# Kernel tuning notes

Measured on AMD Instinct MI355X. Metric: run time of the kernel, lower is better.

Reference implementation:

```python
import jax, jax.numpy as jnp
import numpy as np

N = 10000
E = 160000
IN_DIM = 128
HID = 128
HEADS = 8
INT_DIM = 512
OUT_DIM = 3
NEG_SLOPE = 0.2


def gat_conv(x, src, dst, W, a_src, a_dst, b, heads, ch):
    # x: [N, F_in]; W: [F_in, heads*ch]; a_src/a_dst: [heads, ch]; b: [heads*ch]
    n = x.shape[0]
    h = (x @ W).reshape(n, heads, ch)                      # [N,H,C]
    alpha_src = jnp.einsum('nhc,hc->nh', h, a_src)         # [N,H]
    alpha_dst = jnp.einsum('nhc,hc->nh', h, a_dst)         # [N,H]
    e = jax.nn.leaky_relu(alpha_src[src] + alpha_dst[dst], NEG_SLOPE)  # [E,H]
    # segment softmax over incoming edges of each dst node
    emax = jax.ops.segment_max(e, dst, num_segments=n)     # [N,H]
    ee = jnp.exp(e - emax[dst])
    denom = jax.ops.segment_sum(ee, dst, num_segments=n)   # [N,H]
    alpha = ee / (denom[dst] + 1e-16)                      # [E,H]
    msg = h[src] * alpha[:, :, None]                       # [E,H,C]
    out = jax.ops.segment_sum(msg, dst, num_segments=n)    # [N,H,C]
    return out.reshape(n, heads * ch) + b


def setup_inputs() -> dict:
    key = jax.random.key(0)
    ks = jax.random.split(key, 20)

    def glorot(k, shape):
        fan = shape[0] + shape[-1]
        s = jnp.sqrt(6.0 / fan)
        return jax.random.uniform(k, shape, jnp.float32, -s, s)

    x = jax.random.normal(ks[0], (N, IN_DIM), jnp.float32)
    edge_index = jax.random.randint(ks[1], (2, E), 0, N, jnp.int32)
    return {
        'x': x,
        'edge_index': edge_index,
        'W1': glorot(ks[2], (IN_DIM, HEADS * HID)),
        'a_src1': glorot(ks[3], (HEADS, HID)),
        'a_dst1': glorot(ks[4], (HEADS, HID)),
        'b1': jnp.zeros((HEADS * HID,), jnp.float32),
        'W2': glorot(ks[5], (HEADS * HID, HEADS * HID)),
        'a_src2': glorot(ks[6], (HEADS, HID)),
        'a_dst2': glorot(ks[7], (HEADS, HID)),
        'b2': jnp.zeros((HEADS * HID,), jnp.float32),
        'W3': glorot(ks[8], (HEADS * HID, INT_DIM)),
        'a_src3': glorot(ks[9], (1, INT_DIM)),
        'a_dst3': glorot(ks[10], (1, INT_DIM)),
        'b3': jnp.zeros((INT_DIM,), jnp.float32),
        'Wl': glorot(ks[11], (INT_DIM, INT_DIM)),
        'bl': jnp.zeros((INT_DIM,), jnp.float32),
        'Wc': glorot(ks[12], (INT_DIM, OUT_DIM)),
        'bc': jnp.zeros((OUT_DIM,), jnp.float32),
    }


def reference(x, edge_index, W1, a_src1, a_dst1, b1, W2, a_src2, a_dst2, b2,
              W3, a_src3, a_dst3, b3, Wl, bl, Wc, bc):
    src, dst = edge_index[0], edge_index[1]
    # eval mode: dropout_edge and Dropout are identity
    h = gat_conv(x, src, dst, W1, a_src1, a_dst1, b1, HEADS, HID)
    h = jax.nn.relu(h)
    h = gat_conv(h, src, dst, W2, a_src2, a_dst2, b2, HEADS, HID)
    h = jax.nn.relu(h)
    h = gat_conv(h, src, dst, W3, a_src3, a_dst3, b3, 1, INT_DIM)
    h = jax.nn.relu(h)
    h = jax.nn.relu(h @ Wl + bl)
    return h @ Wc + bc
```

## Files before the change

kernel.cpp:

```cpp
#include <hip/hip_runtime.h>
#include <hip/hip_bf16.h>

#define NN 10000
#define EE 160000
#define IN_DIM 128
#define HID 128
#define HEADS 8
#define F1 (HEADS*HID)
#define INT_DIM 512
#define OUT_DIM 3
#define MPAD 10112

typedef __attribute__((ext_vector_type(4))) float f32x4;
typedef __attribute__((ext_vector_type(8))) _Float16 half8;
typedef __attribute__((ext_vector_type(4))) _Float16 half4;
typedef __attribute__((ext_vector_type(2))) _Float16 half2v;

#define WAVE_SYNC() do { asm volatile("s_waitcnt lgkmcnt(0)" ::: "memory"); \
                         __builtin_amdgcn_sched_barrier(0); } while(0)

__global__ __launch_bounds__(256) void count_kernel(const int* __restrict__ dst, int E, int* __restrict__ cnt){
    int e = blockIdx.x*256 + threadIdx.x;
    if(e < E) atomicAdd(&cnt[dst[e]], 1);
}

__global__ __launch_bounds__(256) void scan_kernel(const int* __restrict__ cnt, int* __restrict__ rowp,
                                                   int* __restrict__ cursor, int n){
    __shared__ int sh[256];
    __shared__ int stotal;
    int t = threadIdx.x;
    if(t==0) stotal = 0;
    __syncthreads();
    for(int base=0; base<n; base+=256){
        int i = base + t;
        int v = (i<n) ? cnt[i] : 0;
        sh[t] = v;
        __syncthreads();
        #pragma unroll
        for(int off=1; off<256; off<<=1){
            int add = (t>=off) ? sh[t-off] : 0;
            __syncthreads();
            sh[t] += add;
            __syncthreads();
        }
        int excl = sh[t] - v;
        if(i<n){ rowp[i] = stotal + excl; cursor[i] = stotal + excl; }
        int chunk_total = sh[255];
        __syncthreads();
        if(t==0) stotal += chunk_total;
        __syncthreads();
    }
    if(t==0) rowp[n] = stotal;
}

__global__ __launch_bounds__(256) void fill_kernel(const int* __restrict__ src, const int* __restrict__ dst,
                                                   int E, int* __restrict__ cursor, int* __restrict__ colsrc){
    int e = blockIdx.x*256 + threadIdx.x;
    if(e < E){
        int d = dst[e];
        int pos = atomicAdd(&cursor[d], 1);
        colsrc[pos] = src[e];
    }
}

__global__ __launch_bounds__(256) void splitT16_kernel(const float* __restrict__ B, _Float16* __restrict__ T,
                                                       int K, int N){
    __shared__ float tile[32][33];
    const int tx = threadIdx.x & 31, ty = threadIdx.x >> 5;
    const int n0 = blockIdx.x * 32, k0 = blockIdx.y * 32;
    #pragma unroll
    for(int i = 0; i < 32; i += 8)
        tile[ty + i][tx] = B[(size_t)(k0 + ty + i) * N + n0 + tx];
    __syncthreads();
    #pragma unroll
    for(int i = 0; i < 32; i += 8){
        int n = ty + i;
        T[(size_t)(n0 + n) * K + k0 + tx] = (_Float16)tile[tx][n];
    }
}

__global__ __launch_bounds__(256) void x16_kernel(const float* __restrict__ x, _Float16* __restrict__ x16, int n4){
    int i = blockIdx.x*256 + threadIdx.x;
    if(i >= n4) return;
    float4 v = ((const float4*)x)[i];
    half4 o = { (_Float16)v.x, (_Float16)v.y, (_Float16)v.z, (_Float16)v.w };
    ((half4*)x16)[i] = o;
}

__global__ __launch_bounds__(256) void aw1_kernel(const float* __restrict__ W1,
                                                  const float* __restrict__ a_src,
                                                  const float* __restrict__ a_dst,
                                                  float* __restrict__ aw){
    int idx = blockIdx.x*256 + threadIdx.x;
    if(idx >= 16*IN_DIM) return;
    int j = idx >> 7, k = idx & 127;
    int hj = j & 7;
    const float* av = (j < 8 ? a_src : a_dst) + hj*HID;
    const float* wr = W1 + (size_t)k*F1 + hj*HID;
    float s = 0.f;
    #pragma unroll 4
    for(int c = 0; c < HID; c++) s += av[c] * wr[c];
    aw[idx] = s;
}

__global__ __launch_bounds__(256) void alpha1_kernel(const float* __restrict__ x,
                                                     const float* __restrict__ aw,
                                                     float* __restrict__ asrc, float* __restrict__ adst){
    __shared__ float xs[16][128];
    __shared__ float aws[16][128];
    int t = threadIdx.x;
    int nb = blockIdx.x * 16;
    for(int i = t; i < 16*128; i += 256){
        xs[i >> 7][i & 127] = x[(size_t)nb*128 + i];
        aws[i >> 7][i & 127] = aw[i];
    }
    __syncthreads();
    int nl = t >> 4, j = t & 15;
    float s = 0.f;
    #pragma unroll 4
    for(int c = 0; c < 128; c++) s += xs[nl][c] * aws[j][c];
    int node = nb + nl;
    if(j < 8) asrc[node*8 + j] = s;
    else      adst[node*8 + (j-8)] = s;
}

__global__ __launch_bounds__(256) void agg1_kernel(const _Float16* __restrict__ x16,
                                                   const float* __restrict__ asrc,
                                                   const float* __restrict__ adst,
                                                   const int* __restrict__ rowp,
                                                   const int* __restrict__ colsrc,
                                                   _Float16* __restrict__ oa){
    const int w = threadIdx.x >> 6, l = threadIdx.x & 63;
    const int node = blockIdx.x*4 + w;
    __shared__ float sh_ee[4][64][8];
    int beg = rowp[node], end = rowp[node+1];
    float rd = adst[node*8 + (l & 7)];
    float acc0[8], acc1[8];
    #pragma unroll
    for(int h=0;h<8;h++){ acc0[h]=0.f; acc1[h]=0.f; }
    float dpart = 0.f;
    for(int base=beg; base<end; base+=64){
        int clen = min(64, end-base);
        WAVE_SYNC();
        int sreg = (l < clen) ? colsrc[base + l] : 0;
        for(int it=l; it<clen*8; it+=64){
            int j = it >> 3;
            int s = colsrc[base + j];
            float e = asrc[s*8 + (l & 7)] + rd;
            e = (e > 0.f) ? e : 0.2f*e;
            float ee = expf(e);
            sh_ee[w][j][l & 7] = ee;
            dpart += ee;
        }
        WAVE_SYNC();
        #pragma unroll 2
        for(int j=0;j<clen;j++){
            int s = __shfl(sreg, j);
            half2v xv = ((const half2v*)(x16 + (size_t)s*128))[l];
            float x0 = (float)xv[0], x1 = (float)xv[1];
            #pragma unroll
            for(int h=0;h<8;h++){
                float wt = sh_ee[w][j][h];
                acc0[h] += wt * x0;
                acc1[h] += wt * x1;
            }
        }
    }
    dpart += __shfl_xor(dpart, 8);
    dpart += __shfl_xor(dpart, 16);
    dpart += __shfl_xor(dpart, 32);
    #pragma unroll
    for(int h=0;h<8;h++){
        float dn = __shfl(dpart, h) + 1e-16f;
        half2v o = { (_Float16)(acc0[h]/dn), (_Float16)(acc1[h]/dn) };
        *(half2v*)(oa + (size_t)node*F1 + h*128 + 2*l) = o;
    }
}

__device__ inline void fma8x2(float* acc, half8 v0, half8 v1, float w0, float w1){
    #pragma unroll
    for(int k=0;k<8;k++){
        acc[k]   += w0 * (float)v0[k];
        acc[8+k] += w1 * (float)v1[k];
    }
}
__device__ inline void fma8(float* acc, half8 v, float w){
    #pragma unroll
    for(int k=0;k<8;k++) acc[k] += w * (float)v[k];
}

__global__ __launch_bounds__(256) void agg2_kernel(const _Float16* __restrict__ hbuf,
                                                   const float* __restrict__ asrc,
                                                   const float* __restrict__ adst,
                                                   const int* __restrict__ rowp,
                                                   const int* __restrict__ colsrc,
                                                   const float* __restrict__ bias,
                                                   _Float16* __restrict__ oa){
    const int w = threadIdx.x >> 6, l = threadIdx.x & 63;
    const int node = blockIdx.x*4 + w;
    __shared__ float sh_ee[4][64][8];
    int beg = rowp[node], end = rowp[node+1];
    float rd = adst[node*8 + (l & 7)];
    float acc[16];
    #pragma unroll
    for(int k=0;k<16;k++) acc[k]=0.f;
    float dpart = 0.f;
    for(int base=beg; base<end; base+=64){
        int clen = min(64, end-base);
        int cpad = (clen + 3) & ~3;
        WAVE_SYNC();
        int sreg = (l < clen) ? colsrc[base + l] : 0;
        #pragma unroll 1
        for(int it=l; it<cpad*8; it+=64){
            int j = it >> 3;
            float ee = 0.f;
            if(j < clen){
                int s = colsrc[base + j];
                float e = asrc[s*8 + (l & 7)] + rd;
                e = (e > 0.f) ? e : 0.2f*e;
                ee = expf(e);
                dpart += ee;
            }
            sh_ee[w][j][l & 7] = ee;
        }
        WAVE_SYNC();
        int sA=__shfl(sreg,0), sB=__shfl(sreg,1), sC=__shfl(sreg,2), sD=__shfl(sreg,3);
        const half8* pA=(const half8*)(hbuf+(size_t)sA*F1);
        const half8* pB=(const half8*)(hbuf+(size_t)sB*F1);
        const half8* pC=(const half8*)(hbuf+(size_t)sC*F1);
        const half8* pD=(const half8*)(hbuf+(size_t)sD*F1);
        half8 vA0=pA[l], vA1=pA[l+64];
        half8 vB0=pB[l], vB1=pB[l+64];
        half8 vC0=pC[l], vC1=pC[l+64];
        half8 vD0=pD[l], vD1=pD[l+64];
        const int h0 = l>>4, h1 = 4 + (l>>4);
        #pragma unroll 1
        for(int j0=0; j0<cpad; j0+=4){
            half8 nA0,nA1,nB0,nB1,nC0,nC1,nD0,nD1;
            const bool more = (j0+4 < cpad);
            if(more){
                int t0=__shfl(sreg,j0+4), t1=__shfl(sreg,j0+5), t2=__shfl(sreg,j0+6), t3=__shfl(sreg,j0+7);
                const half8* q0=(const half8*)(hbuf+(size_t)t0*F1);
                const half8* q1=(const half8*)(hbuf+(size_t)t1*F1);
                const half8* q2=(const half8*)(hbuf+(size_t)t2*F1);
                const half8* q3=(const half8*)(hbuf+(size_t)t3*F1);
                nA0=q0[l]; nA1=q0[l+64];
                nB0=q1[l]; nB1=q1[l+64];
                nC0=q2[l]; nC1=q2[l+64];
                nD0=q3[l]; nD1=q3[l+64];
            }
            fma8x2(acc, vA0, vA1, sh_ee[w][j0  ][h0], sh_ee[w][j0  ][h1]);
            fma8x2(acc, vB0, vB1, sh_ee[w][j0+1][h0], sh_ee[w][j0+1][h1]);
            fma8x2(acc, vC0, vC1, sh_ee[w][j0+2][h0], sh_ee[w][j0+2][h1]);
            fma8x2(acc, vD0, vD1, sh_ee[w][j0+3][h0], sh_ee[w][j0+3][h1]);
            if(more){
                vA0=nA0; vA1=nA1; vB0=nB0; vB1=nB1;
                vC0=nC0; vC1=nC1; vD0=nD0; vD1=nD1;
            }
        }
    }
    dpart += __shfl_xor(dpart, 8);
    dpart += __shfl_xor(dpart, 16);
    dpart += __shfl_xor(dpart, 32);
    float dn0 = __shfl(dpart, l>>4) + 1e-16f;
    float dn1 = __shfl(dpart, 4 + (l>>4)) + 1e-16f;
    const float4* bp = (const float4*)bias;
    float4 ba0 = bp[2*l],       ba1 = bp[2*l+1];
    float4 bc0 = bp[128 + 2*l], bc1 = bp[128 + 2*l+1];
    float bb0[8] = {ba0.x,ba0.y,ba0.z,ba0.w, ba1.x,ba1.y,ba1.z,ba1.w};
    float bb1[8] = {bc0.x,bc0.y,bc0.z,bc0.w, bc1.x,bc1.y,bc1.z,bc1.w};
    half8 o0, o1;
    #pragma unroll
    for(int k=0;k<8;k++){
        o0[k] = (_Float16)fmaxf(acc[k]/dn0 + bb0[k], 0.f);
        o1[k] = (_Float16)fmaxf(acc[8+k]/dn1 + bb1[k], 0.f);
    }
    size_t off0 = (size_t)node*F1 + 8*l;
    *(half8*)(oa + off0) = o0;
    *(half8*)(oa + off0 + 512) = o1;
}

__global__ __launch_bounds__(256) void agg3_kernel(const _Float16* __restrict__ hbuf,
                                                   const float* __restrict__ asrc,
                                                   const float* __restrict__ adst,
                                                   const int* __restrict__ rowp,
                                                   const int* __restrict__ colsrc,
                                                   const float* __restrict__ bias,
                                                   _Float16* __restrict__ oa){
    const int w = threadIdx.x >> 6, l = threadIdx.x & 63;
    const int node = blockIdx.x*4 + w;
    int beg = rowp[node], end = rowp[node+1];
    float rd = adst[node];
    float acc[8];
    #pragma unroll
    for(int k=0;k<8;k++) acc[k]=0.f;
    float dpart = 0.f;
    for(int base=beg; base<end; base+=64){
        int clen = min(64, end-base);
        int sreg = 0; float eereg = 0.f;
        if(l < clen){
            sreg = colsrc[base + l];
            float e = asrc[sreg] + rd;
            e = (e > 0.f) ? e : 0.2f*e;
            eereg = expf(e);
            dpart += eereg;
        }
        int cpad = (clen + 7) & ~7;
        half8 v[8];
        float wt[8];
        #pragma unroll
        for(int k=0;k<8;k++){
            int s = __shfl(sreg, k);
            wt[k] = __shfl(eereg, k);
            v[k] = ((const half8*)(hbuf + (size_t)s*INT_DIM))[l];
        }
        #pragma unroll 1
        for(int j0=0; j0<cpad; j0+=8){
            half8 nv[8]; float nw[8];
            const bool more = (j0+8 < cpad);
            if(more){
                #pragma unroll
                for(int k=0;k<8;k++){
                    int s = __shfl(sreg, j0+8+k);
                    nw[k] = __shfl(eereg, j0+8+k);
                    nv[k] = ((const half8*)(hbuf + (size_t)s*INT_DIM))[l];
                }
            }
            #pragma unroll
            for(int k=0;k<8;k++) fma8(acc, v[k], wt[k]);
            if(more){
                #pragma unroll
                for(int k=0;k<8;k++){ v[k]=nv[k]; wt[k]=nw[k]; }
            }
        }
    }
    #pragma unroll
    for(int off=1; off<64; off<<=1) dpart += __shfl_xor(dpart, off);
    float dn = dpart + 1e-16f;
    const float4* bp = (const float4*)bias;
    float4 ba0 = bp[2*l], ba1 = bp[2*l+1];
    float bb[8] = {ba0.x,ba0.y,ba0.z,ba0.w, ba1.x,ba1.y,ba1.z,ba1.w};
    half8 o;
    #pragma unroll
    for(int k=0;k<8;k++)
        o[k] = (_Float16)fmaxf(acc[k]/dn + bb[k], 0.f);
    *(half8*)(oa + (size_t)node*INT_DIM + 8*l) = o;
}

template<int FUSE>
__global__ __launch_bounds__(512, 4) void mfma16_gemm_kernel(
    const _Float16* __restrict__ A, int lda, int za,
    const _Float16* __restrict__ B, int ldb, int zb,
    const float* __restrict__ bias, _Float16* __restrict__ O,
    int ldc, int zc, int K, int gx)
{
    __shared__ _Float16 lA[2][128*32];
    __shared__ _Float16 lB[2][128*32];
    const int tid  = threadIdx.x;
    const int lane = tid & 63;
    const int w    = tid >> 6;
    const int wm   = w >> 2;
    const int wn   = w & 3;
    const int z    = blockIdx.z;

    const int nwg = gridDim.x;
    const int q = nwg >> 3, r = nwg & 7;
    const int xcd = blockIdx.x & 7, idx = blockIdx.x >> 3;
    const int wgid = (xcd < r ? xcd*(q+1) : r*(q+1) + (xcd-r)*q) + idx;
    const int row0 = (wgid / gx) * 128, col0 = (wgid % gx) * 128;

    f32x4 acc[4][2];
    #pragma unroll
    for(int i=0;i<4;i++)
        #pragma unroll
        for(int j=0;j<2;j++) acc[i][j] = (f32x4){0.f,0.f,0.f,0.f};

    const int rr1 = tid >> 2;
    const int ss1 = (tid & 3) ^ ((rr1 >> 1) & 3);
    const size_t aoff = (size_t)(row0 + rr1) * lda + (size_t)z*za + ss1 * 8;
    const size_t boff = (size_t)(col0 + rr1) * ldb + (size_t)z*zb + ss1 * 8;

    typedef __attribute__((address_space(3))) char lds_char;
    lds_char* dA = (lds_char*)(&lA[0][0]) + w*1024;
    lds_char* dB = (lds_char*)(&lB[0][0]) + w*1024;

    int arow[4], brow[2];
    const int slotx = ((lane >> 4) ^ ((lane >> 1) & 3)) << 4;
    #pragma unroll
    for(int i=0;i<4;i++)
        arow[i] = (wm*64 + i*16 + (lane & 15)) * 64 + slotx;
    #pragma unroll
    for(int j=0;j<2;j++)
        brow[j] = (wn*32 + j*16 + (lane & 15)) * 64 + slotx;

    #define GLDS(src, dst) __builtin_amdgcn_global_load_lds( \
        (__attribute__((address_space(1))) void*)(src), \
        (__attribute__((address_space(3))) void*)(dst), 16, 0, 0)
    GLDS(A + aoff, dA);
    GLDS(B + boff, dB);
    __syncthreads();

    #pragma unroll 1
    for(int k0 = 0, kb = 0; k0 < K; k0 += 32, kb ^= 1){
        if(k0 + 32 < K){
            const int nb = kb ^ 1;
            GLDS(A + aoff + k0 + 32, dA + nb*8192);
            GLDS(B + boff + k0 + 32, dB + nb*8192);
        }
        const char* pA = (const char*)(&lA[0][0]) + kb*8192;
        const char* pB = (const char*)(&lB[0][0]) + kb*8192;
        half8 af[4];
        #pragma unroll
        for(int i=0;i<4;i++) af[i] = *(const half8*)(pA + arow[i]);
        #pragma unroll
        for(int j=0;j<2;j++){
            half8 bf = *(const half8*)(pB + brow[j]);
            #pragma unroll
            for(int i=0;i<4;i++)
                acc[i][j] = __builtin_amdgcn_mfma_f32_16x16x32_f16(af[i], bf, acc[i][j], 0, 0, 0);
        }
        __syncthreads();
    }
    #undef GLDS

    #pragma unroll
    for(int i=0;i<4;i++){
        const int rr = row0 + wm*64 + i*16 + ((lane >> 4) << 2);
        #pragma unroll
        for(int j=0;j<2;j++){
            const int gc = z*zc + col0 + wn*32 + j*16 + (lane & 15);
            float b = FUSE ? bias[gc] : 0.f;
            #pragma unroll
            for(int rg=0;rg<4;rg++){
                float v = acc[i][j][rg];
                if(FUSE) v = fmaxf(v + b, 0.f);
                O[(size_t)(rr + rg) * ldc + gc] = (_Float16)v;
            }
        }
    }
}

__global__ __launch_bounds__(128) void alpha16_h8_kernel(const _Float16* __restrict__ hbuf,
                                                         const float* __restrict__ a_src,
                                                         const float* __restrict__ a_dst,
                                                         float* __restrict__ asrc, float* __restrict__ adst){
    int node = blockIdx.x;
    int t = threadIdx.x;
    half8 v = ((const half8*)(hbuf + (size_t)node*F1))[t];
    const float4* ap = (const float4*)(a_src + 8*t);
    const float4* dp = (const float4*)(a_dst + 8*t);
    float4 a0 = ap[0], a1 = ap[1];
    float4 d0 = dp[0], d1 = dp[1];
    float av[8] = {a0.x,a0.y,a0.z,a0.w, a1.x,a1.y,a1.z,a1.w};
    float dv[8] = {d0.x,d0.y,d0.z,d0.w, d1.x,d1.y,d1.z,d1.w};
    float ps = 0.f, pd = 0.f;
    #pragma unroll
    for(int k=0;k<8;k++){
        float f = (float)v[k];
        ps += f * av[k];
        pd += f * dv[k];
    }
    #pragma unroll
    for(int off=8; off; off>>=1){ ps += __shfl_down(ps, off); pd += __shfl_down(pd, off); }
    if((t & 15) == 0){
        asrc[(size_t)node*8 + (t>>4)] = ps;
        adst[(size_t)node*8 + (t>>4)] = pd;
    }
}

__global__ __launch_bounds__(128) void alpha16_h1_kernel(const _Float16* __restrict__ hbuf,
                                                         const float* __restrict__ a_src,
                                                         const float* __restrict__ a_dst,
                                                         float* __restrict__ asrc, float* __restrict__ adst){
    int node = blockIdx.x;
    int t = threadIdx.x;
    half4 v = ((const half4*)(hbuf + (size_t)node*INT_DIM))[t];
    float4 a = ((const float4*)a_src)[t];
    float4 d = ((const float4*)a_dst)[t];
    float ps = (float)v[0]*a.x + (float)v[1]*a.y + (float)v[2]*a.z + (float)v[3]*a.w;
    float pd = (float)v[0]*d.x + (float)v[1]*d.y + (float)v[2]*d.z + (float)v[3]*d.w;
    #pragma unroll
    for(int off=32; off; off>>=1){ ps += __shfl_down(ps, off); pd += __shfl_down(pd, off); }
    __shared__ float shs[2], shd[2];
    int wv = t >> 6;
    if((t & 63) == 0){ shs[wv] = ps; shd[wv] = pd; }
    __syncthreads();
    if(t == 0){
        asrc[node] = shs[0] + shs[1];
        adst[node] = shd[0] + shd[1];
    }
}

__global__ __launch_bounds__(256) void cls16_kernel(const _Float16* __restrict__ h, const float* __restrict__ Wc,
                                                    const float* __restrict__ bc, float* __restrict__ out, int n){
    int node = blockIdx.x*4 + (threadIdx.x >> 6);
    int lane = threadIdx.x & 63;
    if(node >= n) return;
    half8 v = ((const half8*)(h + (size_t)node*INT_DIM))[lane];
    float s0=0.f, s1=0.f, s2=0.f;
    #pragma unroll
    for(int k=0;k<8;k++){
        float f = (float)v[k];
        const float* wr = Wc + (8*lane + k)*3;
        s0 += f * wr[0];
        s1 += f * wr[1];
        s2 += f * wr[2];
    }
    #pragma unroll
    for(int off=32; off; off>>=1){
        s0 += __shfl_down(s0, off);
        s1 += __shfl_down(s1, off);
        s2 += __shfl_down(s2, off);
    }
    if(lane==0){
        out[(size_t)node*3+0] = s0 + bc[0];
        out[(size_t)node*3+1] = s1 + bc[1];
        out[(size_t)node*3+2] = s2 + bc[2];
    }
}

extern "C" void kernel_launch(void* const* d_in, const int* in_sizes, int n_in,
                              void* d_out, int out_size, void* d_ws, size_t ws_size,
                              hipStream_t stream){
    const float* x      = (const float*)d_in[0];
    const int*   ei     = (const int*)d_in[1];
    const float* W1     = (const float*)d_in[2];
    const float* a_src1 = (const float*)d_in[3];
    const float* a_dst1 = (const float*)d_in[4];
    const float* b1     = (const float*)d_in[5];
    const float* W2     = (const float*)d_in[6];
    const float* a_src2 = (const float*)d_in[7];
    const float* a_dst2 = (const float*)d_in[8];
    const float* b2     = (const float*)d_in[9];
    const float* W3     = (const float*)d_in[10];
    const float* a_src3 = (const float*)d_in[11];
    const float* a_dst3 = (const float*)d_in[12];
    const float* b3     = (const float*)d_in[13];
    const float* Wl     = (const float*)d_in[14];
    const float* bl     = (const float*)d_in[15];
    const float* Wc     = (const float*)d_in[16];
    const float* bc     = (const float*)d_in[17];
    float* out = (float*)d_out;

    const int* src = ei;
    const int* dst = ei + EE;

    char* p = (char*)d_ws;
    char* regA = p;  p += (size_t)MPAD*F1*4;
    char* regB = p;  p += (size_t)MPAD*F1*4;
    _Float16* wt16 = (_Float16*)p;  p += (size_t)F1*F1*2;
    _Float16* x16  = (_Float16*)p;  p += (size_t)NN*IN_DIM*2;
    float* aw1  = (float*)p;  p += 16*IN_DIM*4;
    float* asrc = (float*)p;  p += (size_t)NN*HEADS*4;
    float* adst = (float*)p;  p += (size_t)NN*HEADS*4;
    int* cnt    = (int*)p;    p += NN*4;
    int* rowp   = (int*)p;    p += (NN+1)*4;
    int* cursor = (int*)p;    p += NN*4;
    int* colsrc = (int*)p;    p += EE*4;

    _Float16* hA = (_Float16*)regA;
    _Float16* hB = (_Float16*)regB;

    hipMemsetAsync(cnt, 0, NN*sizeof(int), stream);
    count_kernel<<<(EE+255)/256, 256, 0, stream>>>(dst, EE, cnt);
    scan_kernel<<<1, 256, 0, stream>>>(cnt, rowp, cursor, NN);
    fill_kernel<<<(EE+255)/256, 256, 0, stream>>>(src, dst, EE, cursor, colsrc);

    x16_kernel<<<(NN*IN_DIM/4 + 255)/256, 256, 0, stream>>>(x, x16, NN*IN_DIM/4);
    splitT16_kernel<<<dim3(F1/32, IN_DIM/32), 256, 0, stream>>>(W1, wt16, IN_DIM, F1);
    aw1_kernel<<<8, 256, 0, stream>>>(W1, a_src1, a_dst1, aw1);
    alpha1_kernel<<<NN/16, 256, 0, stream>>>(x, aw1, asrc, adst);
    agg1_kernel<<<NN/4, 256, 0, stream>>>(x16, asrc, adst, rowp, colsrc, hA);
    mfma16_gemm_kernel<1><<<dim3(MPAD/128, 1, HEADS), 512, 0, stream>>>(
        hA, F1, 128,  wt16, IN_DIM, 128*IN_DIM,
        b1, hB, F1, 128,  IN_DIM, 1);

    splitT16_kernel<<<dim3(F1/32, F1/32), 256, 0, stream>>>(W2, wt16, F1, F1);
    mfma16_gemm_kernel<0><<<dim3((F1/128)*(MPAD/128), 1, 1), 512, 0, stream>>>(
        hB, F1, 0,  wt16, F1, 0,
        nullptr, hA, F1, 0,  F1, F1/128);
    alpha16_h8_kernel<<<NN, 128, 0, stream>>>(hA, a_src2, a_dst2, asrc, adst);
    agg2_kernel<<<NN/4, 256, 0, stream>>>(hA, asrc, adst, rowp, colsrc, b2, hB);

    splitT16_kernel<<<dim3(INT_DIM/32, F1/32), 256, 0, stream>>>(W3, wt16, F1, INT_DIM);
    mfma16_gemm_kernel<0><<<dim3((INT_DIM/128)*(MPAD/128), 1, 1), 512, 0, stream>>>(
        hB, F1, 0,  wt16, F1, 0,
        nullptr, hA, INT_DIM, 0,  F1, INT_DIM/128);
    alpha16_h1_kernel<<<NN, 128, 0, stream>>>(hA, a_src3, a_dst3, asrc, adst);
    agg3_kernel<<<NN/4, 256, 0, stream>>>(hA, asrc, adst, rowp, colsrc, b3, hB);

    splitT16_kernel<<<dim3(INT_DIM/32, INT_DIM/32), 256, 0, stream>>>(Wl, wt16, INT_DIM, INT_DIM);
    mfma16_gemm_kernel<1><<<dim3((INT_DIM/128)*(MPAD/128), 1, 1), 512, 0, stream>>>(
        hB, INT_DIM, 0,  wt16, INT_DIM, 0,
        bl, hA, INT_DIM, 0,  INT_DIM, INT_DIM/128);

    cls16_kernel<<<(NN+3)/4, 256, 0, stream>>>(hA, Wc, bc, out, NN);
}
```

Measured before the change: 297.5 us.

## Split agg2/agg3 aggregation across feature chunks per block for more parallelism

The layer-2 and layer-3 aggregation kernels now assign one 128-feature chunk (a head for agg2, a quarter of the 512 features for agg3) to each block, and each lane handles two features. This launches eight times as many waves, which gives more memory-level parallelism for the gather-bound neighbour loads and cuts per-thread register use. In exchange, the edge-score computation (colsrc, asrc, exp) is repeated once per chunk, and each gather load shrinks to 4 bytes per lane, which may lower per-request efficiency.

```diff
diff --git a/kernel.cpp b/kernel.cpp
--- a/kernel.cpp
+++ b/kernel.cpp
@@ -177,18 +177,6 @@
     }
 }
 
-__device__ inline void fma8x2(float* acc, half8 v0, half8 v1, float w0, float w1){
-    #pragma unroll
-    for(int k=0;k<8;k++){
-        acc[k]   += w0 * (float)v0[k];
-        acc[8+k] += w1 * (float)v1[k];
-    }
-}
-__device__ inline void fma8(float* acc, half8 v, float w){
-    #pragma unroll
-    for(int k=0;k<8;k++) acc[k] += w * (float)v[k];
-}
-
 __global__ __launch_bounds__(256) void agg2_kernel(const _Float16* __restrict__ hbuf,
                                                    const float* __restrict__ asrc,
                                                    const float* __restrict__ adst,
@@ -197,87 +185,62 @@
                                                    const float* __restrict__ bias,
                                                    _Float16* __restrict__ oa){
     const int w = threadIdx.x >> 6, l = threadIdx.x & 63;
-    const int node = blockIdx.x*4 + w;
-    __shared__ float sh_ee[4][64][8];
+    const int h = blockIdx.x & 7;
+    const int node = (blockIdx.x >> 3)*4 + w;
     int beg = rowp[node], end = rowp[node+1];
-    float rd = adst[node*8 + (l & 7)];
-    float acc[16];
-    #pragma unroll
-    for(int k=0;k<16;k++) acc[k]=0.f;
+    float rd = adst[node*8 + h];
+    float acc0 = 0.f, acc1 = 0.f;
     float dpart = 0.f;
+    const _Float16* hb = hbuf + h*128 + 2*l;
     for(int base=beg; base<end; base+=64){
         int clen = min(64, end-base);
-        int cpad = (clen + 3) & ~3;
-        WAVE_SYNC();
-        int sreg = (l < clen) ? colsrc[base + l] : 0;
+        int sreg = 0; float eereg = 0.f;
+        if(l < clen){
+            sreg = colsrc[base + l];
+            float e = asrc[sreg*8 + h] + rd;
+            e = (e > 0.f) ? e : 0.2f*e;
+            eereg = expf(e);
+            dpart += eereg;
+        }
+        int cpad = (clen + 7) & ~7;
+        half2v v[8]; float wt[8];
+        #pragma unroll
+        for(int k=0;k<8;k++){
+            int s = __shfl(sreg, k);
+            wt[k] = __shfl(eereg, k);
+            v[k] = *(const half2v*)(hb + (size_t)s*F1);
+        }
         #pragma unroll 1
-        for(int it=l; it<cpad*8; it+=64){
-            int j = it >> 3;
-            float ee = 0.f;
-            if(j < clen){
-                int s = colsrc[base + j];
-                float e = asrc[s*8 + (l & 7)] + rd;
-                e = (e > 0.f) ? e : 0.2f*e;
-                ee = expf(e);
-                dpart += ee;
-            }
-            sh_ee[w][j][l & 7] = ee;
-        }
-        WAVE_SYNC();
-        int sA=__shfl(sreg,0), sB=__shfl(sreg,1), sC=__shfl(sreg,2), sD=__shfl(sreg,3);
-        const half8* pA=(const half8*)(hbuf+(size_t)sA*F1);
-        const half8* pB=(const half8*)(hbuf+(size_t)sB*F1);
-        const half8* pC=(const half8*)(hbuf+(size_t)sC*F1);
-        const half8* pD=(const half8*)(hbuf+(size_t)sD*F1);
-        half8 vA0=pA[l], vA1=pA[l+64];
-        half8 vB0=pB[l], vB1=pB[l+64];
-        half8 vC0=pC[l], vC1=pC[l+64];
-        half8 vD0=pD[l], vD1=pD[l+64];
-        const int h0 = l>>4, h1 = 4 + (l>>4);
-        #pragma unroll 1
-        for(int j0=0; j0<cpad; j0+=4){
-            half8 nA0,nA1,nB0,nB1,nC0,nC1,nD0,nD1;
-            const bool more = (j0+4 < cpad);
+        for(int j0=0; j0<cpad; j0+=8){
+            half2v nv[8]; float nw[8];
+            const bool more = (j0+8 < cpad);
             if(more){
-                int t0=__shfl(sreg,j0+4), t1=__shfl(sreg,j0+5), t2=__shfl(sreg,j0+6), t3=__shfl(sreg,j0+7);
-                const half8* q0=(const half8*)(hbuf+(size_t)t0*F1);
-                const half8* q1=(const half8*)(hbuf+(size_t)t1*F1);
-                const half8* q2=(const half8*)(hbuf+(size_t)t2*F1);
-                const half8* q3=(const half8*)(hbuf+(size_t)t3*F1);
-                nA0=q0[l]; nA1=q0[l+64];
-                nB0=q1[l]; nB1=q1[l+64];
-                nC0=q2[l]; nC1=q2[l+64];
-                nD0=q3[l]; nD1=q3[l+64];
-            }
-            fma8x2(acc, vA0, vA1, sh_ee[w][j0  ][h0], sh_ee[w][j0  ][h1]);
-            fma8x2(acc, vB0, vB1, sh_ee[w][j0+1][h0], sh_ee[w][j0+1][h1]);
-            fma8x2(acc, vC0, vC1, sh_ee[w][j0+2][h0], sh_ee[w][j0+2][h1]);
-            fma8x2(acc, vD0, vD1, sh_ee[w][j0+3][h0], sh_ee[w][j0+3][h1]);
+                #pragma unroll
+                for(int k=0;k<8;k++){
+                    int s = __shfl(sreg, j0+8+k);
+                    nw[k] = __shfl(eereg, j0+8+k);
+                    nv[k] = *(const half2v*)(hb + (size_t)s*F1);
+                }
+            }
+            #pragma unroll
+            for(int k=0;k<8;k++){
+                acc0 += wt[k]*(float)v[k][0];
+                acc1 += wt[k]*(float)v[k][1];
+            }
             if(more){
-                vA0=nA0; vA1=nA1; vB0=nB0; vB1=nB1;
-                vC0=nC0; vC1=nC1; vD0=nD0; vD1=nD1;
-            }
-        }
-    }
-    dpart += __shfl_xor(dpart, 8);
-    dpart += __shfl_xor(dpart, 16);
-    dpart += __shfl_xor(dpart, 32);
-    float dn0 = __shfl(dpart, l>>4) + 1e-16f;
-    float dn1 = __shfl(dpart, 4 + (l>>4)) + 1e-16f;
-    const float4* bp = (const float4*)bias;
-    float4 ba0 = bp[2*l],       ba1 = bp[2*l+1];
-    float4 bc0 = bp[128 + 2*l], bc1 = bp[128 + 2*l+1];
-    float bb0[8] = {ba0.x,ba0.y,ba0.z,ba0.w, ba1.x,ba1.y,ba1.z,ba1.w};
-    float bb1[8] = {bc0.x,bc0.y,bc0.z,bc0.w, bc1.x,bc1.y,bc1.z,bc1.w};
-    half8 o0, o1;
-    #pragma unroll
-    for(int k=0;k<8;k++){
-        o0[k] = (_Float16)fmaxf(acc[k]/dn0 + bb0[k], 0.f);
-        o1[k] = (_Float16)fmaxf(acc[8+k]/dn1 + bb1[k], 0.f);
-    }
-    size_t off0 = (size_t)node*F1 + 8*l;
-    *(half8*)(oa + off0) = o0;
-    *(half8*)(oa + off0 + 512) = o1;
+                #pragma unroll
+                for(int k=0;k<8;k++){ v[k]=nv[k]; wt[k]=nw[k]; }
+            }
+        }
+    }
+    #pragma unroll
+    for(int off=1; off<64; off<<=1) dpart += __shfl_xor(dpart, off);
+    float dn = dpart + 1e-16f;
+    const int f = h*128 + 2*l;
+    float2 bb = *(const float2*)(bias + f);
+    half2v o = { (_Float16)fmaxf(acc0/dn + bb.x, 0.f),
+                 (_Float16)fmaxf(acc1/dn + bb.y, 0.f) };
+    *(half2v*)(oa + (size_t)node*F1 + f) = o;
 }
 
 __global__ __launch_bounds__(256) void agg3_kernel(const _Float16* __restrict__ hbuf,
@@ -288,13 +251,14 @@
                                                    const float* __restrict__ bias,
                                                    _Float16* __restrict__ oa){
     const int w = threadIdx.x >> 6, l = threadIdx.x & 63;
-    const int node = blockIdx.x*4 + w;
+    const int i = blockIdx.x & 7;
+    const int chunk = i & 3, sub = i >> 2;
+    const int node = ((blockIdx.x >> 3)*2 + sub)*4 + w;
     int beg = rowp[node], end = rowp[node+1];
     float rd = adst[node];
-    float acc[8];
-    #pragma unroll
-    for(int k=0;k<8;k++) acc[k]=0.f;
+    float acc0 = 0.f, acc1 = 0.f;
     float dpart = 0.f;
+    const _Float16* hb = hbuf + chunk*128 + 2*l;
     for(int base=beg; base<end; base+=64){
         int clen = min(64, end-base);
         int sreg = 0; float eereg = 0.f;
@@ -306,28 +270,30 @@
             dpart += eereg;
         }
         int cpad = (clen + 7) & ~7;
-        half8 v[8];
-        float wt[8];
+        half2v v[8]; float wt[8];
         #pragma unroll
         for(int k=0;k<8;k++){
             int s = __shfl(sreg, k);
             wt[k] = __shfl(eereg, k);
-            v[k] = ((const half8*)(hbuf + (size_t)s*INT_DIM))[l];
+            v[k] = *(const half2v*)(hb + (size_t)s*INT_DIM);
         }
         #pragma unroll 1
         for(int j0=0; j0<cpad; j0+=8){
-            half8 nv[8]; float nw[8];
+            half2v nv[8]; float nw[8];
             const bool more = (j0+8 < cpad);
             if(more){
                 #pragma unroll
                 for(int k=0;k<8;k++){
                     int s = __shfl(sreg, j0+8+k);
                     nw[k] = __shfl(eereg, j0+8+k);
-                    nv[k] = ((const half8*)(hbuf + (size_t)s*INT_DIM))[l];
+                    nv[k] = *(const half2v*)(hb + (size_t)s*INT_DIM);
                 }
             }
             #pragma unroll
-            for(int k=0;k<8;k++) fma8(acc, v[k], wt[k]);
+            for(int k=0;k<8;k++){
+                acc0 += wt[k]*(float)v[k][0];
+                acc1 += wt[k]*(float)v[k][1];
+            }
             if(more){
                 #pragma unroll
                 for(int k=0;k<8;k++){ v[k]=nv[k]; wt[k]=nw[k]; }
@@ -337,14 +303,11 @@
     #pragma unroll
     for(int off=1; off<64; off<<=1) dpart += __shfl_xor(dpart, off);
     float dn = dpart + 1e-16f;
-    const float4* bp = (const float4*)bias;
-    float4 ba0 = bp[2*l], ba1 = bp[2*l+1];
-    float bb[8] = {ba0.x,ba0.y,ba0.z,ba0.w, ba1.x,ba1.y,ba1.z,ba1.w};
-    half8 o;
-    #pragma unroll
-    for(int k=0;k<8;k++)
-        o[k] = (_Float16)fmaxf(acc[k]/dn + bb[k], 0.f);
-    *(half8*)(oa + (size_t)node*INT_DIM + 8*l) = o;
+    const int f = chunk*128 + 2*l;
+    float2 bb = *(const float2*)(bias + f);
+    half2v o = { (_Float16)fmaxf(acc0/dn + bb.x, 0.f),
+                 (_Float16)fmaxf(acc1/dn + bb.y, 0.f) };
+    *(half2v*)(oa + (size_t)node*INT_DIM + f) = o;
 }
 
 template<int FUSE>
@@ -580,14 +543,14 @@
         hB, F1, 0,  wt16, F1, 0,
         nullptr, hA, F1, 0,  F1, F1/128);
     alpha16_h8_kernel<<<NN, 128, 0, stream>>>(hA, a_src2, a_dst2, asrc, adst);
-    agg2_kernel<<<NN/4, 256, 0, stream>>>(hA, asrc, adst, rowp, colsrc, b2, hB);
+    agg2_kernel<<<(NN/4)*8, 256, 0, stream>>>(hA, asrc, adst, rowp, colsrc, b2, hB);
 
     splitT16_kernel<<<dim3(INT_DIM/32, F1/32), 256, 0, stream>>>(W3, wt16, F1, INT_DIM);
     mfma16_gemm_kernel<0><<<dim3((INT_DIM/128)*(MPAD/128), 1, 1), 512, 0, stream>>>(
         hB, F1, 0,  wt16, F1, 0,
         nullptr, hA, INT_DIM, 0,  F1, INT_DIM/128);
     alpha16_h1_kernel<<<NN, 128, 0, stream>>>(hA, a_src3, a_dst3, asrc, adst);
-    agg3_kernel<<<NN/4, 256, 0, stream>>>(hA, asrc, adst, rowp, colsrc, b3, hB);
+    agg3_kernel<<<(NN/8)*8, 256, 0, stream>>>(hA, asrc, adst, rowp, colsrc, b3, hB);
 
     splitT16_kernel<<<dim3(INT_DIM/32, INT_DIM/32), 256, 0, stream>>>(Wl, wt16, INT_DIM, INT_DIM);
     mfma16_gemm_kernel<1><<<dim3((INT_DIM/128)*(MPAD/128), 1, 1), 512, 0, stream>>>(
```

Measured after the change: 299.4 us. About the same (+0.6%).
